# Kernel optimization log

Hardware: AMD Instinct MI355X
Metric: run time of the kernel (lower is better)

## Reference

```python
import jax, jax.numpy as jnp
import numpy as np

D_MODEL = 1024
N_HEADS = 16
HEAD_DIM = D_MODEL // N_HEADS


def setup_inputs() -> dict:
    key = jax.random.key(0)
    ks = jax.random.split(key, 5)
    B, T = 4, 4096
    x = jax.random.normal(ks[0], (B, T, D_MODEL), dtype=jnp.float32)
    s = 1.0 / np.sqrt(D_MODEL)
    Wqkv = jax.random.normal(ks[1], (D_MODEL, 3 * D_MODEL), dtype=jnp.float32) * s
    bqkv = jnp.zeros((3 * D_MODEL,), dtype=jnp.float32)
    Wout = jax.random.normal(ks[2], (D_MODEL, D_MODEL), dtype=jnp.float32) * s
    bout = jnp.zeros((D_MODEL,), dtype=jnp.float32)
    return {"x": x, "Wqkv": Wqkv, "bqkv": bqkv, "Wout": Wout, "bout": bout}


def _feature_map(x):
    # elu(x) + 1  (strictly positive feature map)
    return jax.nn.elu(x) + 1.0


def reference(x, Wqkv, bqkv, Wout, bout):
    B, T, C = x.shape
    H, D = N_HEADS, HEAD_DIM
    qkv = x @ Wqkv + bqkv                      # [B,T,3C]
    qkv = qkv.reshape(B, T, 3, H, D)
    qkv = jnp.transpose(qkv, (2, 0, 3, 1, 4))  # [3,B,H,T,D]
    q, k, v = qkv[0], qkv[1], qkv[2]
    scale = D ** 0.25
    q_m = _feature_map(q / scale)
    k_m = _feature_map(k / scale)
    kv = jnp.einsum('bhtd,bhtm->bhdm', k_m, v)     # [B,H,D,D]
    out = jnp.einsum('bhtd,bhdm->bhtm', q_m, kv)   # [B,H,T,D]
    z = q_m.sum(axis=-1, keepdims=True)            # note: sum over feature dim (as in source)
    out = out / (z + 1e-6)
    out = jnp.transpose(out, (0, 2, 1, 3)).reshape(B, T, C)
    return out @ Wout + bout
```

## Files before the change

### kernel.cpp

```cpp
#include <hip/hip_runtime.h>
#include <hip/hip_bf16.h>
#include <math.h>

#define B_ 4
#define T_ 4096
#define H_ 16
#define D_ 64
#define C_ 1024
#define BT_ (B_*T_)

using short8  = __attribute__((ext_vector_type(8))) short;
using floatx4 = __attribute__((ext_vector_type(4))) float;

__device__ __forceinline__ float feature_map(float x) {
    return x > 0.0f ? x + 1.0f : __expf(x);
}
__device__ __forceinline__ unsigned short f2bf(float x) {
    union { __hip_bfloat16 b; unsigned short u; } c;
    c.b = __float2bfloat16(x);
    return c.u;
}
__device__ __forceinline__ void async16(const void* g, void* l) {
    __builtin_amdgcn_global_load_lds(
        (const __attribute__((address_space(1))) void*)g,
        (__attribute__((address_space(3))) void*)l, 16, 0, 0);
}
__device__ __forceinline__ const char* sel3(const char* a0, const char* a1,
                                            const char* a2, int t) {
    return t == 0 ? a0 : (t == 1 ? a1 : a2);
}

__global__ __launch_bounds__(256)
void convert_x_kernel(const float4* __restrict__ x, ushort* __restrict__ xb)
{
    const size_t n = (size_t)BT_ * C_ / 8;
    for (size_t i = (size_t)blockIdx.x * 256 + threadIdx.x; i < n;
         i += (size_t)2048 * 256) {
        const float4 a = x[2 * i], b = x[2 * i + 1];
        short8 r;
        r[0] = (short)f2bf(a.x); r[1] = (short)f2bf(a.y);
        r[2] = (short)f2bf(a.z); r[3] = (short)f2bf(a.w);
        r[4] = (short)f2bf(b.x); r[5] = (short)f2bf(b.y);
        r[6] = (short)f2bf(b.z); r[7] = (short)f2bf(b.w);
        *reinterpret_cast<short8*>(&xb[i * 8]) = r;
    }
}

__global__ __launch_bounds__(256)
void transpose_w_kernel(const float* __restrict__ Wqkv, ushort* __restrict__ WqkvT,
                        const float* __restrict__ Wout, ushort* __restrict__ WoutT)
{
    __shared__ float t[32][33];
    const bool qkv = blockIdx.x < 96;
    const float* W  = qkv ? Wqkv : Wout;
    ushort* WT      = qkv ? WqkvT : WoutT;
    const int N     = qkv ? 3 * C_ : C_;
    const int n0 = (qkv ? blockIdx.x : blockIdx.x - 96) * 32, k0 = blockIdx.y * 32;
    const int r = threadIdx.x >> 5, c = threadIdx.x & 31;
    #pragma unroll
    for (int i = 0; i < 4; i++)
        t[r + 8 * i][c] = W[(size_t)(k0 + r + 8 * i) * N + n0 + c];
    __syncthreads();
    #pragma unroll
    for (int i = 0; i < 4; i++)
        WT[(size_t)(n0 + r + 8 * i) * C_ + k0 + c] = f2bf(t[c][r + 8 * i]);
}

#define BAR()    __builtin_amdgcn_s_barrier()
#define WAITDS() do { asm volatile("s_waitcnt lgkmcnt(0)" ::: "memory"); \
                      __builtin_amdgcn_sched_barrier(0); } while(0)
#define VM6()    do { asm volatile("s_waitcnt vmcnt(6)" ::: "memory"); \
                      __builtin_amdgcn_sched_barrier(0); } while(0)

#define LDA(slot, mf, ks, buf) \
    aR[slot][ks] = *(const short8*)(smem + (buf)*32768 + ((mf)>>2)*16384 + \
                                    aRowB + ((mf)&3)*2048 + cks##ks)
#define LDB(nf, ks, buf) \
    bR[nf][ks] = *(const short8*)(smem + 65536 + (buf)*32768 + ((nf)>>1)*16384 + \
                                  bRowB + ((nf)&1)*2048 + cks##ks)
#define LDA8(MB, BUF) do { \
    LDA(0, MB+0, 0, BUF); LDA(0, MB+0, 1, BUF); \
    LDA(1, MB+1, 0, BUF); LDA(1, MB+1, 1, BUF); \
    LDA(2, MB+2, 0, BUF); LDA(2, MB+2, 1, BUF); \
    LDA(3, MB+3, 0, BUF); LDA(3, MB+3, 1, BUF); } while(0)
#define LDB4(NF, BUF) do { \
    LDB(NF+0, 0, BUF); LDB(NF+0, 1, BUF); \
    LDB(NF+1, 0, BUF); LDB(NF+1, 1, BUF); } while(0)

#define MM(mf, nf, ks, slot) \
    acc[mf][nf] = __builtin_amdgcn_mfma_f32_16x16x32_bf16( \
        aR[slot][ks], bR[nf][ks], acc[mf][nf], 0, 0, 0)
#define MFMAQ(MB, NF) do { \
    MM(MB+0,NF+0,0,0); MM(MB+1,NF+0,0,1); MM(MB+2,NF+0,0,2); MM(MB+3,NF+0,0,3); \
    MM(MB+0,NF+1,0,0); MM(MB+1,NF+1,0,1); MM(MB+2,NF+1,0,2); MM(MB+3,NF+1,0,3); \
    MM(MB+0,NF+0,1,0); MM(MB+1,NF+0,1,1); MM(MB+2,NF+0,1,2); MM(MB+3,NF+0,1,3); \
    MM(MB+0,NF+1,1,0); MM(MB+1,NF+1,1,1); MM(MB+2,NF+1,1,2); MM(MB+3,NF+1,1,3); \
} while(0)

#define STGA(h, G, buf) do { int _g = (G); if (_g >= NTILE*16) _g -= NTILE*16; \
    const char* _b = sel3(Ab0, Ab1, Ab2, _g >> 4); const int _w = (_g & 15) * 128; \
    async16(_b + aOf##h##0 + _w, smem + (buf)*32768 + (h)*16384 + wv*1024); \
    async16(_b + aOf##h##1 + _w, smem + (buf)*32768 + (h)*16384 + 8192 + wv*1024); \
} while(0)
#define STGB(h, G, buf) do { int _g = (G); if (_g >= NTILE*16) _g -= NTILE*16; \
    const char* _b = sel3(Bb0, Bb1, Bb2, _g >> 4); const int _w = (_g & 15) * 128; \
    async16(_b + bOf##h##0 + _w, smem + 65536 + (buf)*32768 + (h)*16384 + wv*1024); \
    async16(_b + bOf##h##1 + _w, smem + 65536 + (buf)*32768 + (h)*16384 + 8192 + wv*1024); \
} while(0)

#define ITERBODY(GB) \
    const int g1 = (GB) + 2*it + 1, g2 = (GB) + 2*it + 2, g3 = (GB) + 2*it + 3; \
     BAR(); LDA8(0, 0); LDB4(0, 0); STGA(1, g1, 1); \
    WAITDS(); __builtin_amdgcn_s_setprio(1); MFMAQ(0, 0); \
    __builtin_amdgcn_s_setprio(0); \
     BAR(); LDB4(2, 0); STGA(0, g2, 0); \
    WAITDS(); __builtin_amdgcn_s_setprio(1); MFMAQ(0, 2); \
    __builtin_amdgcn_s_setprio(0); \
     BAR(); LDA8(4, 0); STGB(0, g2, 0); \
    WAITDS(); __builtin_amdgcn_s_setprio(1); MFMAQ(4, 2); \
    __builtin_amdgcn_s_setprio(0); \
     BAR(); STGB(1, g2, 0); \
    WAITDS(); __builtin_amdgcn_s_setprio(1); MFMAQ(4, 0); \
    __builtin_amdgcn_s_setprio(0); VM6(); \
     BAR(); LDA8(0, 1); LDB4(0, 1); STGA(1, g2, 0); \
    WAITDS(); __builtin_amdgcn_s_setprio(1); MFMAQ(0, 0); \
    __builtin_amdgcn_s_setprio(0); \
     BAR(); LDB4(2, 1); STGA(0, g3, 1); \
    WAITDS(); __builtin_amdgcn_s_setprio(1); MFMAQ(0, 2); \
    __builtin_amdgcn_s_setprio(0); \
     BAR(); LDA8(4, 1); STGB(0, g3, 1); \
    WAITDS(); __builtin_amdgcn_s_setprio(1); MFMAQ(4, 2); \
    __builtin_amdgcn_s_setprio(0); \
     BAR(); STGB(1, g3, 1); \
    WAITDS(); __builtin_amdgcn_s_setprio(1); MFMAQ(4, 0); \
    __builtin_amdgcn_s_setprio(0); VM6();

template<int EPI>
__device__ __forceinline__ void gemm_epilogue(
    floatx4 (&acc)[8][4], const float (&bv)[4],
    int mBase, int nBase, int wm, int wn, int lr, int quad,
    ushort* __restrict__ q_out, ushort* __restrict__ kT_out,
    ushort* __restrict__ vT_out, float* __restrict__ f_out)
{
    if (EPI == 0) {
        const float inv_scale = 0.35355339059327373f;
        const int seg = nBase >> 10;
        if (seg == 0) {
            #pragma unroll
            for (int mf = 0; mf < 8; mf++)
                #pragma unroll
                for (int i = 0; i < 4; i++) {
                    float f0 = feature_map((acc[mf][0][i] + bv[0]) * inv_scale);
                    float f1 = feature_map((acc[mf][1][i] + bv[1]) * inv_scale);
                    float f2 = feature_map((acc[mf][2][i] + bv[2]) * inv_scale);
                    float f3 = feature_map((acc[mf][3][i] + bv[3]) * inv_scale);
                    float z = f0 + f1 + f2 + f3;
                    z += __shfl_xor(z, 1); z += __shfl_xor(z, 2);
                    z += __shfl_xor(z, 4); z += __shfl_xor(z, 8);
                    const float inv = 1.0f / (z + 1e-6f);
                    const int t = mBase + wm * 128 + mf * 16 + quad * 4 + i;
                    const int cbase = nBase + wn * 64 + lr;
                    q_out[(size_t)t * C_ + cbase]      = f2bf(f0 * inv);
                    q_out[(size_t)t * C_ + cbase + 16] = f2bf(f1 * inv);
                    q_out[(size_t)t * C_ + cbase + 32] = f2bf(f2 * inv);
                    q_out[(size_t)t * C_ + cbase + 48] = f2bf(f3 * inv);
                }
        } else {
            ushort* dstT = (seg == 1) ? kT_out : vT_out;
            #pragma unroll
            for (int nf = 0; nf < 4; nf++) {
                const int c = (nBase + wn * 64 + nf * 16 + lr) & 1023;
                #pragma unroll
                for (int mf = 0; mf < 8; mf++) {
                    float v0 = acc[mf][nf][0] + bv[nf], v1 = acc[mf][nf][1] + bv[nf];
                    float v2 = acc[mf][nf][2] + bv[nf], v3 = acc[mf][nf][3] + bv[nf];
                    if (seg == 1) {
                        v0 = feature_map(v0 * inv_scale); v1 = feature_map(v1 * inv_scale);
                        v2 = feature_map(v2 * inv_scale); v3 = feature_map(v3 * inv_scale);
                    }
                    const int tt = mBase + wm * 128 + mf * 16 + quad * 4;
                    *(ushort4*)&dstT[(size_t)c * BT_ + tt] =
                        make_ushort4(f2bf(v0), f2bf(v1), f2bf(v2), f2bf(v3));
                }
            }
        }
    } else {
        #pragma unroll
        for (int nf = 0; nf < 4; nf++) {
            const int c = nBase + wn * 64 + nf * 16 + lr;
            #pragma unroll
            for (int mf = 0; mf < 8; mf++)
                #pragma unroll
                for (int i = 0; i < 4; i++) {
                    const int row = mBase + wm * 128 + mf * 16 + quad * 4 + i;
                    f_out[(size_t)row * C_ + c] = acc[mf][nf][i] + bv[nf];
                }
        }
    }
    #pragma unroll
    for (int i = 0; i < 8; i++)
        #pragma unroll
        for (int j = 0; j < 4; j++) acc[i][j] = (floatx4)0.0f;
}

template<int EPI, int NBX, int NTILE>
__device__ __forceinline__ void gemm_body(
    const ushort* __restrict__ A, const ushort* __restrict__ Bm,
    const float* __restrict__ bias,
    ushort* __restrict__ q_out, ushort* __restrict__ kT_out,
    ushort* __restrict__ vT_out, float* __restrict__ f_out)
{
    __shared__ __align__(16) unsigned char smem[131072];

    const int tid = threadIdx.x;
    const int wv = tid >> 6, l = tid & 63;
    const int wm = wv >> 2, wn = wv & 3;
    const int lr = l & 15, quad = l >> 4;

    int mB0, mB1, mB2, nB0, nB1, nB2;
    {
        const int tot = (int)gridDim.x * NTILE, cpx = tot >> 3;
        int lg0 = blockIdx.x;
        int w0 = (lg0 & 7) * cpx + (lg0 >> 3);
        mB0 = (w0 / NBX) * 256; nB0 = (w0 % NBX) * 256;
        if (NTILE > 1) {
            int lg1 = blockIdx.x + (int)gridDim.x;
            int w1 = (lg1 & 7) * cpx + (lg1 >> 3);
            mB1 = (w1 / NBX) * 256; nB1 = (w1 % NBX) * 256;
            int lg2 = blockIdx.x + 2 * (int)gridDim.x;
            int w2 = (lg2 & 7) * cpx + (lg2 >> 3);
            mB2 = (w2 / NBX) * 256; nB2 = (w2 % NBX) * 256;
        } else { mB1 = mB0; nB1 = nB0; mB2 = mB0; nB2 = nB0; }
    }
    const size_t bOffB = (EPI == 1) ? (size_t)(mB0 >> 12) * ((size_t)C_ * C_) : 0;
    const char* Ab0 = (const char*)(A + (size_t)mB0 * C_);
    const char* Ab1 = (const char*)(A + (size_t)mB1 * C_);
    const char* Ab2 = (const char*)(A + (size_t)mB2 * C_);
    const char* Bb0 = (const char*)(Bm + bOffB + (size_t)nB0 * C_);
    const char* Bb1 = (const char*)(Bm + bOffB + (size_t)nB1 * C_);
    const char* Bb2 = (const char*)(Bm + bOffB + (size_t)nB2 * C_);

    float bv0[4], bv1[4], bv2[4];
    #pragma unroll
    for (int nf = 0; nf < 4; nf++) {
        bv0[nf] = bias[nB0 + wn * 64 + nf * 16 + lr];
        bv1[nf] = (NTILE > 1) ? bias[nB1 + wn * 64 + nf * 16 + lr] : bv0[nf];
        bv2[nf] = (NTILE > 1) ? bias[nB2 + wn * 64 + nf * 16 + lr] : bv0[nf];
    }

    const int s0 = tid >> 3;
    const int cb = ((tid & 7) * 16) ^ ((s0 & 7) << 4);
    const int aOf00 = (s0)       * 2048 + cb;
    const int aOf01 = (128 + s0) * 2048 + cb;
    const int aOf10 = (64 + s0)  * 2048 + cb;
    const int aOf11 = (192 + s0) * 2048 + cb;
    const int bq    = (s0 >> 5) * 64 + (s0 & 31);
    const int bOf00 = (bq)       * 2048 + cb;
    const int bOf01 = (bq + 128) * 2048 + cb;
    const int bOf10 = (bq + 32)  * 2048 + cb;
    const int bOf11 = (bq + 160) * 2048 + cb;

    const int aRowB = (wm * 64 + lr) * 128;
    const int bRowB = (wn * 32 + lr) * 128;
    const int cks0 = (quad * 16) ^ ((lr & 7) << 4);
    const int cks1 = 64 ^ cks0;

    floatx4 acc[8][4];
    #pragma unroll
    for (int i = 0; i < 8; i++)
        #pragma unroll
        for (int j = 0; j < 4; j++) acc[i][j] = (floatx4)0.0f;
    short8 aR[4][2], bR[4][2];

    STGA(0, 0, 0); STGB(0, 0, 0); STGB(1, 0, 0); STGA(1, 0, 0);
    STGA(0, 1, 1); STGB(0, 1, 1); STGB(1, 1, 1);
    asm volatile("s_waitcnt vmcnt(6)" ::: "memory");
    __builtin_amdgcn_sched_barrier(0);

    #pragma unroll 1
    for (int it = 0; it < 8; ++it) { ITERBODY(0) }
    gemm_epilogue<EPI>(acc, bv0, mB0, nB0, wm, wn, lr, quad,
                       q_out, kT_out, vT_out, f_out);
    if (NTILE > 1) {
        #pragma unroll 1
        for (int it = 0; it < 8; ++it) { ITERBODY(16) }
        gemm_epilogue<EPI>(acc, bv1, mB1, nB1, wm, wn, lr, quad,
                           q_out, kT_out, vT_out, f_out);
        #pragma unroll 1
        for (int it = 0; it < 8; ++it) { ITERBODY(32) }
        gemm_epilogue<EPI>(acc, bv2, mB2, nB2, wm, wn, lr, quad,
                           q_out, kT_out, vT_out, f_out);
    }
    asm volatile("s_waitcnt vmcnt(0)" ::: "memory");
}

__global__ __launch_bounds__(512, 2)
void qkv8_kernel(const ushort* __restrict__ A, const ushort* __restrict__ Bm,
                 const float* __restrict__ bias, ushort* __restrict__ q_out,
                 ushort* __restrict__ kT_out, ushort* __restrict__ vT_out)
{
    gemm_body<0, 12, 3>(A, Bm, bias, q_out, kT_out, vT_out, nullptr);
}

__global__ __launch_bounds__(512, 2)
void outproj8_kernel(const ushort* __restrict__ A, const ushort* __restrict__ Bm,
                     const float* __restrict__ bias, float* __restrict__ f_out)
{
    gemm_body<1, 4, 1>(A, Bm, bias, nullptr, nullptr, nullptr, f_out);
}

__global__ __launch_bounds__(256)
void kv_accum_kernel(const ushort* __restrict__ kmT, const ushort* __restrict__ vT,
                     float* __restrict__ kv)
{
    const int tid = threadIdx.x;
    const int w = tid >> 6, l = tid & 63;
    const int wm = w >> 1, wn = w & 1;
    const int lr = l & 15, quad = l >> 4;
    const int bh = blockIdx.y;
    const int b = bh >> 4, h = bh & 15;
    const size_t t0 = (size_t)b * T_ + (size_t)blockIdx.x * 256;

    const ushort* Ar = kmT + (size_t)(h * 64 + wm * 32 + lr) * BT_ + t0 + quad * 8;
    const ushort* Br = vT  + (size_t)(h * 64 + wn * 32 + lr) * BT_ + t0 + quad * 8;

    floatx4 acc[2][2];
    #pragma unroll
    for (int i = 0; i < 2; i++)
        #pragma unroll
        for (int j = 0; j < 2; j++) acc[i][j] = (floatx4)0.0f;

    #pragma unroll
    for (int tt = 0; tt < 256; tt += 32) {
        const short8 af0 = *(const short8*)&Ar[tt];
        const short8 af1 = *(const short8*)&Ar[(size_t)16 * BT_ + tt];
        const short8 bf0 = *(const short8*)&Br[tt];
        const short8 bf1 = *(const short8*)&Br[(size_t)16 * BT_ + tt];
        acc[0][0] = __builtin_amdgcn_mfma_f32_16x16x32_bf16(af0, bf0, acc[0][0], 0, 0, 0);
        acc[0][1] = __builtin_amdgcn_mfma_f32_16x16x32_bf16(af0, bf1, acc[0][1], 0, 0, 0);
        acc[1][0] = __builtin_amdgcn_mfma_f32_16x16x32_bf16(af1, bf0, acc[1][0], 0, 0, 0);
        acc[1][1] = __builtin_amdgcn_mfma_f32_16x16x32_bf16(af1, bf1, acc[1][1], 0, 0, 0);
    }

    float* kvb = kv + (size_t)bh * (D_ * D_);
    #pragma unroll
    for (int i = 0; i < 2; i++)
        #pragma unroll
        for (int j = 0; j < 2; j++)
            #pragma unroll
            for (int r = 0; r < 4; r++) {
                const int d = wm * 32 + i * 16 + quad * 4 + r;
                const int m = wn * 32 + j * 16 + lr;
                atomicAdd(&kvb[d * 64 + m], acc[i][j][r]);
            }
}

__global__ __launch_bounds__(256)
void kw_kernel(const float* __restrict__ kv, const ushort* __restrict__ WoutT,
               ushort* __restrict__ KWT)
{
    const int tid = threadIdx.x;
    const int w = tid >> 6, l = tid & 63;
    const int lr = l & 15, quad = l >> 4;
    const int bh = blockIdx.y, b = bh >> 4, h = bh & 15;
    const int c0 = blockIdx.x * 256 + w * 64;

    const float* kvb = kv + (size_t)bh * (D_ * D_);

    short8 bf[4][2];
    #pragma unroll
    for (int df = 0; df < 4; df++)
        #pragma unroll
        for (int ks = 0; ks < 2; ks++) {
            const float* src = &kvb[(df * 16 + lr) * 64 + ks * 32 + quad * 8];
            const float4 u0 = *(const float4*)src;
            const float4 u1 = *(const float4*)(src + 4);
            short8 t;
            t[0] = (short)f2bf(u0.x); t[1] = (short)f2bf(u0.y);
            t[2] = (short)f2bf(u0.z); t[3] = (short)f2bf(u0.w);
            t[4] = (short)f2bf(u1.x); t[5] = (short)f2bf(u1.y);
            t[6] = (short)f2bf(u1.z); t[7] = (short)f2bf(u1.w);
            bf[df][ks] = t;
        }

    floatx4 acc[4][4];
    #pragma unroll
    for (int i = 0; i < 4; i++)
        #pragma unroll
        for (int j = 0; j < 4; j++) acc[i][j] = (floatx4)0.0f;

    #pragma unroll
    for (int ks = 0; ks < 2; ks++) {
        short8 af[4];
        #pragma unroll
        for (int cf = 0; cf < 4; cf++)
            af[cf] = *(const short8*)&WoutT[(size_t)(c0 + cf * 16 + lr) * C_
                                            + h * 64 + ks * 32 + quad * 8];
        #pragma unroll
        for (int cf = 0; cf < 4; cf++)
            #pragma unroll
            for (int df = 0; df < 4; df++)
                acc[cf][df] = __builtin_amdgcn_mfma_f32_16x16x32_bf16(
                    af[cf], bf[df][ks], acc[cf][df], 0, 0, 0);
    }

    ushort* dst = KWT + (size_t)b * (C_ * C_);
    #pragma unroll
    for (int cf = 0; cf < 4; cf++)
        #pragma unroll
        for (int i = 0; i < 4; i++) {
            const int c = c0 + cf * 16 + quad * 4 + i;
            #pragma unroll
            for (int df = 0; df < 4; df++)
                dst[(size_t)c * C_ + h * 64 + df * 16 + lr] = f2bf(acc[cf][df][i]);
        }
}

extern "C" void kernel_launch(void* const* d_in, const int* in_sizes, int n_in,
                              void* d_out, int out_size, void* d_ws, size_t ws_size,
                              hipStream_t stream)
{
    const float* x    = (const float*)d_in[0];
    const float* Wqkv = (const float*)d_in[1];
    const float* bqkv = (const float*)d_in[2];
    const float* Wout = (const float*)d_in[3];
    const float* bout = (const float*)d_in[4];
    float* out = (float*)d_out;

    char* ws = (char*)d_ws;
    ushort* xb     = (ushort*)ws;
    ushort* WqkvT  = (ushort*)(ws + 33554432);
    ushort* WoutT  = (ushort*)(ws + 39845888);
    ushort* qs     = (ushort*)(ws + 41943040);
    float*  kv     = (float*) (ws + 75497472);
    ushort* KWT    = (ushort*)ws;
    ushort* kmT    = (ushort*)d_out;
    ushort* vT     = (ushort*)((char*)d_out + 33554432);

    hipMemsetAsync(kv, 0, (size_t)B_ * H_ * D_ * D_ * sizeof(float), stream);

    convert_x_kernel<<<2048, 256, 0, stream>>>((const float4*)x, xb);
    transpose_w_kernel<<<dim3(128, 32), 256, 0, stream>>>(Wqkv, WqkvT, Wout, WoutT);

    qkv8_kernel<<<dim3(256), 512, 0, stream>>>(xb, WqkvT, bqkv, qs, kmT, vT);
    kv_accum_kernel<<<dim3(16, B_ * H_), 256, 0, stream>>>(kmT, vT, kv);
    kw_kernel<<<dim3(4, B_ * H_), 256, 0, stream>>>(kv, WoutT, KWT);
    outproj8_kernel<<<dim3(256), 512, 0, stream>>>(qs, KWT, bout, out);
}
```

Baseline: 311.8 us.

## Merge prep kernels, coarsen GEMM pipeline phases, halve kv_accum grid

Folds the x conversion and the weight transpose into one prep kernel launch, which removes a launch and lets the two jobs overlap. The GEMM main loop now uses 4 barrier phases per iteration instead of 8, issuing more LDS reads and async global-to-LDS stages per phase. This cuts barrier and wait overhead but raises register pressure and leaves less room to overlap loads with MFMAs. kv_accum now gives each block 512 timesteps instead of 256, halving the grid and the atomic accumulations at the cost of fewer blocks in flight.

Result: slower. 326.0 us (+4.6%).

```diff
diff --git a/kernel.cpp b/kernel.cpp
--- a/kernel.cpp
+++ b/kernel.cpp
@@ -31,39 +31,41 @@
 }
 
 __global__ __launch_bounds__(256)
-void convert_x_kernel(const float4* __restrict__ x, ushort* __restrict__ xb)
-{
-    const size_t n = (size_t)BT_ * C_ / 8;
-    for (size_t i = (size_t)blockIdx.x * 256 + threadIdx.x; i < n;
-         i += (size_t)2048 * 256) {
-        const float4 a = x[2 * i], b = x[2 * i + 1];
-        short8 r;
-        r[0] = (short)f2bf(a.x); r[1] = (short)f2bf(a.y);
-        r[2] = (short)f2bf(a.z); r[3] = (short)f2bf(a.w);
-        r[4] = (short)f2bf(b.x); r[5] = (short)f2bf(b.y);
-        r[6] = (short)f2bf(b.z); r[7] = (short)f2bf(b.w);
-        *reinterpret_cast<short8*>(&xb[i * 8]) = r;
-    }
-}
-
-__global__ __launch_bounds__(256)
-void transpose_w_kernel(const float* __restrict__ Wqkv, ushort* __restrict__ WqkvT,
-                        const float* __restrict__ Wout, ushort* __restrict__ WoutT)
+void prep_kernel(const float4* __restrict__ x, ushort* __restrict__ xb,
+                 const float* __restrict__ Wqkv, ushort* __restrict__ WqkvT,
+                 const float* __restrict__ Wout, ushort* __restrict__ WoutT)
 {
     __shared__ float t[32][33];
-    const bool qkv = blockIdx.x < 96;
-    const float* W  = qkv ? Wqkv : Wout;
-    ushort* WT      = qkv ? WqkvT : WoutT;
-    const int N     = qkv ? 3 * C_ : C_;
-    const int n0 = (qkv ? blockIdx.x : blockIdx.x - 96) * 32, k0 = blockIdx.y * 32;
-    const int r = threadIdx.x >> 5, c = threadIdx.x & 31;
-    #pragma unroll
-    for (int i = 0; i < 4; i++)
-        t[r + 8 * i][c] = W[(size_t)(k0 + r + 8 * i) * N + n0 + c];
-    __syncthreads();
-    #pragma unroll
-    for (int i = 0; i < 4; i++)
-        WT[(size_t)(n0 + r + 8 * i) * C_ + k0 + c] = f2bf(t[c][r + 8 * i]);
+    const int bx = blockIdx.x;
+    if (bx < 2048) {
+        const size_t n = (size_t)BT_ * C_ / 8;
+        for (size_t i = (size_t)bx * 256 + threadIdx.x; i < n;
+             i += (size_t)2048 * 256) {
+            const float4 a = x[2 * i], b = x[2 * i + 1];
+            short8 r;
+            r[0] = (short)f2bf(a.x); r[1] = (short)f2bf(a.y);
+            r[2] = (short)f2bf(a.z); r[3] = (short)f2bf(a.w);
+            r[4] = (short)f2bf(b.x); r[5] = (short)f2bf(b.y);
+            r[6] = (short)f2bf(b.z); r[7] = (short)f2bf(b.w);
+            *reinterpret_cast<short8*>(&xb[i * 8]) = r;
+        }
+    } else {
+        const int id = bx - 2048;
+        const int xi = id & 127, y = id >> 7;
+        const bool qkv = xi < 96;
+        const float* W  = qkv ? Wqkv : Wout;
+        ushort* WT      = qkv ? WqkvT : WoutT;
+        const int N     = qkv ? 3 * C_ : C_;
+        const int n0 = (qkv ? xi : xi - 96) * 32, k0 = y * 32;
+        const int r = threadIdx.x >> 5, c = threadIdx.x & 31;
+        #pragma unroll
+        for (int i = 0; i < 4; i++)
+            t[r + 8 * i][c] = W[(size_t)(k0 + r + 8 * i) * N + n0 + c];
+        __syncthreads();
+        #pragma unroll
+        for (int i = 0; i < 4; i++)
+            WT[(size_t)(n0 + r + 8 * i) * C_ + k0 + c] = f2bf(t[c][r + 8 * i]);
+    }
 }
 
 #define BAR()    __builtin_amdgcn_s_barrier()
@@ -110,29 +112,17 @@
 
 #define ITERBODY(GB) \
     const int g1 = (GB) + 2*it + 1, g2 = (GB) + 2*it + 2, g3 = (GB) + 2*it + 3; \
-     BAR(); LDA8(0, 0); LDB4(0, 0); STGA(1, g1, 1); \
-    WAITDS(); __builtin_amdgcn_s_setprio(1); MFMAQ(0, 0); \
+     BAR(); LDA8(0, 0); LDB4(0, 0); LDB4(2, 0); STGA(1, g1, 1); \
+    WAITDS(); __builtin_amdgcn_s_setprio(1); MFMAQ(0, 0); MFMAQ(0, 2); \
     __builtin_amdgcn_s_setprio(0); \
-     BAR(); LDB4(2, 0); STGA(0, g2, 0); \
-    WAITDS(); __builtin_amdgcn_s_setprio(1); MFMAQ(0, 2); \
+     BAR(); LDA8(4, 0); STGA(0, g2, 0); STGB(0, g2, 0); STGB(1, g2, 0); \
+    WAITDS(); __builtin_amdgcn_s_setprio(1); MFMAQ(4, 2); MFMAQ(4, 0); \
+    __builtin_amdgcn_s_setprio(0); VM6(); \
+     BAR(); LDA8(0, 1); LDB4(0, 1); LDB4(2, 1); STGA(1, g2, 0); \
+    WAITDS(); __builtin_amdgcn_s_setprio(1); MFMAQ(0, 0); MFMAQ(0, 2); \
     __builtin_amdgcn_s_setprio(0); \
-     BAR(); LDA8(4, 0); STGB(0, g2, 0); \
-    WAITDS(); __builtin_amdgcn_s_setprio(1); MFMAQ(4, 2); \
-    __builtin_amdgcn_s_setprio(0); \
-     BAR(); STGB(1, g2, 0); \
-    WAITDS(); __builtin_amdgcn_s_setprio(1); MFMAQ(4, 0); \
-    __builtin_amdgcn_s_setprio(0); VM6(); \
-     BAR(); LDA8(0, 1); LDB4(0, 1); STGA(1, g2, 0); \
-    WAITDS(); __builtin_amdgcn_s_setprio(1); MFMAQ(0, 0); \
-    __builtin_amdgcn_s_setprio(0); \
-     BAR(); LDB4(2, 1); STGA(0, g3, 1); \
-    WAITDS(); __builtin_amdgcn_s_setprio(1); MFMAQ(0, 2); \
-    __builtin_amdgcn_s_setprio(0); \
-     BAR(); LDA8(4, 1); STGB(0, g3, 1); \
-    WAITDS(); __builtin_amdgcn_s_setprio(1); MFMAQ(4, 2); \
-    __builtin_amdgcn_s_setprio(0); \
-     BAR(); STGB(1, g3, 1); \
-    WAITDS(); __builtin_amdgcn_s_setprio(1); MFMAQ(4, 0); \
+     BAR(); LDA8(4, 1); STGA(0, g3, 1); STGB(0, g3, 1); STGB(1, g3, 1); \
+    WAITDS(); __builtin_amdgcn_s_setprio(1); MFMAQ(4, 2); MFMAQ(4, 0); \
     __builtin_amdgcn_s_setprio(0); VM6();
 
 template<int EPI>
@@ -319,7 +309,7 @@
     const int lr = l & 15, quad = l >> 4;
     const int bh = blockIdx.y;
     const int b = bh >> 4, h = bh & 15;
-    const size_t t0 = (size_t)b * T_ + (size_t)blockIdx.x * 256;
+    const size_t t0 = (size_t)b * T_ + (size_t)blockIdx.x * 512;
 
     const ushort* Ar = kmT + (size_t)(h * 64 + wm * 32 + lr) * BT_ + t0 + quad * 8;
     const ushort* Br = vT  + (size_t)(h * 64 + wn * 32 + lr) * BT_ + t0 + quad * 8;
@@ -330,8 +320,8 @@
         #pragma unroll
         for (int j = 0; j < 2; j++) acc[i][j] = (floatx4)0.0f;
 
-    #pragma unroll
-    for (int tt = 0; tt < 256; tt += 32) {
+    #pragma unroll 8
+    for (int tt = 0; tt < 512; tt += 32) {
         const short8 af0 = *(const short8*)&Ar[tt];
         const short8 af1 = *(const short8*)&Ar[(size_t)16 * BT_ + tt];
         const short8 bf0 = *(const short8*)&Br[tt];
@@ -439,11 +429,11 @@
 
     hipMemsetAsync(kv, 0, (size_t)B_ * H_ * D_ * D_ * sizeof(float), stream);
 
-    convert_x_kernel<<<2048, 256, 0, stream>>>((const float4*)x, xb);
-    transpose_w_kernel<<<dim3(128, 32), 256, 0, stream>>>(Wqkv, WqkvT, Wout, WoutT);
+    prep_kernel<<<6144, 256, 0, stream>>>((const float4*)x, xb,
+                                          Wqkv, WqkvT, Wout, WoutT);
 
     qkv8_kernel<<<dim3(256), 512, 0, stream>>>(xb, WqkvT, bqkv, qs, kmT, vT);
-    kv_accum_kernel<<<dim3(16, B_ * H_), 256, 0, stream>>>(kmT, vT, kv);
+    kv_accum_kernel<<<dim3(8, B_ * H_), 256, 0, stream>>>(kmT, vT, kv);
     kw_kernel<<<dim3(4, B_ * H_), 256, 0, stream>>>(kv, WoutT, KWT);
     outproj8_kernel<<<dim3(256), 512, 0, stream>>>(qs, KWT, bout, out);
 }
```
